# Performance work log

Hardware: AMD Instinct MI355X
Metric: run time of the kernel (lower is better)

The kernel has to match this reference:

```python
import jax, jax.numpy as jnp
import numpy as np

B, H, W, C = 8, 64, 64, 64
C8 = C // 8

def setup_inputs() -> dict:
    key = jax.random.key(0)
    ks = jax.random.split(key, 5)
    x = jax.random.normal(ks[0], (B, H, W, C), dtype=jnp.float32)
    # 1x1 conv kernels (fan-in scaled) + biases
    wq = jax.random.normal(ks[1], (C, C8), dtype=jnp.float32) / np.sqrt(C)
    wk = jax.random.normal(ks[2], (C, C8), dtype=jnp.float32) / np.sqrt(C)
    wv = jax.random.normal(ks[3], (C, C), dtype=jnp.float32) / np.sqrt(C)
    bq = jnp.zeros((C8,), dtype=jnp.float32)
    bk = jnp.zeros((C8,), dtype=jnp.float32)
    bv = jnp.zeros((C,), dtype=jnp.float32)
    gamma = jax.random.normal(ks[4], (), dtype=jnp.float32)
    return {"x": x, "wq": wq, "bq": bq, "wk": wk, "bk": bk,
            "wv": wv, "bv": bv, "gamma": gamma}

def reference(x, wq, bq, wk, bk, wv, bv, gamma):
    b, h, w, c = x.shape
    n = h * w
    # 1x1 convs == per-pixel linear projections
    q = (jnp.einsum('bhwc,cd->bhwd', x, wq) + bq).reshape(b, n, -1)  # [B,N,C/8]
    k = (jnp.einsum('bhwc,cd->bhwd', x, wk) + bk).reshape(b, n, -1)  # [B,N,C/8]
    v = (jnp.einsum('bhwc,cd->bhwd', x, wv) + bv).reshape(b, n, -1)  # [B,N,C]
    # Unscaled attention: softmax over keys (last axis), no 1/sqrt(d)
    attn = jax.nn.softmax(jnp.einsum('bnd,bmd->bnm', q, k), axis=-1)  # [B,N,N]
    out = jnp.einsum('bnm,bmc->bnc', attn, v).reshape(b, h, w, c)
    return out * gamma + x
```

## Files before the change

### kernel.cpp

```cpp
#include <hip/hip_runtime.h>
#include <hip/hip_bf16.h>


#define BB 8
#define NN 4096
#define CC 64
#define PSTRIDE 72
#define LOG2E 1.44269504088896f

typedef _Float16 f16;
typedef _Float16 half8 __attribute__((ext_vector_type(8)));
typedef _Float16 half4 __attribute__((ext_vector_type(4)));
typedef __fp16 fp16x2 __attribute__((ext_vector_type(2)));
typedef float floatx4 __attribute__((ext_vector_type(4)));

static __device__ inline half4 pack4(float a, float b, float c, float d) {
    fp16x2 lo = __builtin_amdgcn_cvt_pkrtz(a, b);
    fp16x2 hi = __builtin_amdgcn_cvt_pkrtz(c, d);
    unsigned int lou = __builtin_bit_cast(unsigned int, lo);
    unsigned int hiu = __builtin_bit_cast(unsigned int, hi);
    unsigned long long packed = (unsigned long long)lou | ((unsigned long long)hiu << 32);
    return __builtin_bit_cast(half4, packed);
}


__global__ __launch_bounds__(256) void proj_all_kernel(
    const float* __restrict__ x,
    const float* __restrict__ wq, const float* __restrict__ bq,
    const float* __restrict__ wk, const float* __restrict__ bk,
    const float* __restrict__ wv, const float* __restrict__ bv,
    f16* __restrict__ Qh, f16* __restrict__ Kf, f16* __restrict__ Vf,
    float* __restrict__ qn2, float* __restrict__ Mkb)
{
    __shared__ alignas(16) f16 Ws[80][PSTRIDE];
    __shared__ float Bs[80];
    __shared__ alignas(16) f16 Vst[64][68];
    __shared__ alignas(16) f16 Ks[64][12];
    __shared__ float redK[4];
    const int tid = threadIdx.x;

    for (int i4 = tid; i4 < 1024; i4 += 256) {
        const int i = i4 * 4;
        const int cin = i >> 6, cout = i & 63;
        const float4 w = *(const float4*)(wv + i);
        Ws[cout + 0][cin] = (f16)w.x;
        Ws[cout + 1][cin] = (f16)w.y;
        Ws[cout + 2][cin] = (f16)w.z;
        Ws[cout + 3][cin] = (f16)w.w;
    }
    if (tid < 128) {
        const int i = tid * 4;
        const int cin = i >> 3, c = i & 7;
        const float4 a = *(const float4*)(wq + i);
        const float4 k = *(const float4*)(wk + i);
        Ws[64 + c + 0][cin] = (f16)(a.x * LOG2E);
        Ws[64 + c + 1][cin] = (f16)(a.y * LOG2E);
        Ws[64 + c + 2][cin] = (f16)(a.z * LOG2E);
        Ws[64 + c + 3][cin] = (f16)(a.w * LOG2E);
        Ws[72 + c + 0][cin] = (f16)k.x;
        Ws[72 + c + 1][cin] = (f16)k.y;
        Ws[72 + c + 2][cin] = (f16)k.z;
        Ws[72 + c + 3][cin] = (f16)k.w;
    }
    if (tid < 80)
        Bs[tid] = (tid < 64) ? bv[tid]
                : (tid < 72 ? bq[tid - 64] * LOG2E : bk[tid - 72]);
    __syncthreads();

    const int wave = tid >> 6, lane = tid & 63;
    const int quad = lane >> 4, n16 = lane & 15;
    const long pb = (long)blockIdx.x * 64;
    const long p0 = pb + wave * 16;
    const int  b   = (int)(pb >> 12);
    const int  nnb = (int)(pb & 4095);

    half8 ax[2];
#pragma unroll
    for (int kh = 0; kh < 2; ++kh) {
        const float* xp = x + (p0 + n16) * 64 + kh * 32 + quad * 8;
        float4 x1 = *(const float4*)xp;
        float4 x2 = *(const float4*)(xp + 4);
        ax[kh][0] = (f16)x1.x; ax[kh][1] = (f16)x1.y;
        ax[kh][2] = (f16)x1.z; ax[kh][3] = (f16)x1.w;
        ax[kh][4] = (f16)x2.x; ax[kh][5] = (f16)x2.y;
        ax[kh][6] = (f16)x2.z; ax[kh][7] = (f16)x2.w;
    }

#pragma unroll
    for (int ct = 0; ct < 5; ++ct) {
        const int cout = (ct < 4) ? ct * 16 + n16 : 64 + n16;
        const float bias = Bs[cout];
        half8 b0 = *(const half8*)(&Ws[cout][quad * 8]);
        half8 b1 = *(const half8*)(&Ws[cout][32 + quad * 8]);
        floatx4 acc = {bias, bias, bias, bias};
        acc = __builtin_amdgcn_mfma_f32_16x16x32_f16(ax[0], b0, acc, 0, 0, 0);
        acc = __builtin_amdgcn_mfma_f32_16x16x32_f16(ax[1], b1, acc, 0, 0, 0);
        if (ct < 4) {
            half4 vp = {(f16)acc[0], (f16)acc[1], (f16)acc[2], (f16)acc[3]};
            *(half4*)(&Vst[ct * 16 + n16][wave * 16 + quad * 4]) = vp;
        } else {
            float n2[4];
#pragma unroll
            for (int r = 0; r < 4; ++r) n2[r] = acc[r] * acc[r];
#pragma unroll
            for (int d = 1; d < 8; d <<= 1)
#pragma unroll
                for (int r = 0; r < 4; ++r) n2[r] += __shfl_xor(n2[r], d, 64);
            if (n16 == 0) {
#pragma unroll
                for (int r = 0; r < 4; ++r) qn2[p0 + quad * 4 + r] = n2[r];
            }
            float km = fmaxf(fmaxf(n2[0], n2[1]), fmaxf(n2[2], n2[3]));
            km = fmaxf(km, __shfl_xor(km, 16, 64));
            km = fmaxf(km, __shfl_xor(km, 32, 64));
            if (n16 == 8) redK[wave] = km;
            if (n16 < 8) {
                f16* dst = Qh + (p0 + quad * 4) * 8 + n16;
#pragma unroll
                for (int r = 0; r < 4; ++r) dst[r * 8] = (f16)acc[r];
            } else {
#pragma unroll
                for (int r = 0; r < 4; ++r)
                    Ks[wave * 16 + quad * 4 + r][n16 - 8] = (f16)acc[r];
            }
        }
    }
    __syncthreads();

    if (tid == 0) {
        float m = fmaxf(fmaxf(redK[0], redK[1]), fmaxf(redK[2], redK[3]));
        Mkb[blockIdx.x] = m;
    }

#pragma unroll
    for (int u = 0; u < 2; ++u) {
        const int tt = wave * 2 + u;
        const int kb = tt >> 2, ct = tt & 3;
        half4 lo = *(const half4*)(&Vst[ct * 16 + n16][kb * 32 + quad * 4]);
        half4 hi = *(const half4*)(&Vst[ct * 16 + n16][kb * 32 + 16 + quad * 4]);
        half8 v = {lo[0], lo[1], lo[2], lo[3], hi[0], hi[1], hi[2], hi[3]};
        const size_t kbg = (size_t)b * 128 + (nnb >> 5) + kb;
        *(half8*)(Vf + (kbg * 4 + ct) * 512 + lane * 8) = v;
    }
    if (wave < 2) {
        half8 kp = {0, 0, 0, 0, 0, 0, 0, 0};
#pragma unroll
        for (int e = 0; e < 2; ++e) {
            const int t = wave * 2 + e;
            if (quad < 2) {
                half4 kd = *(const half4*)(&Ks[t * 16 + n16][quad * 4]);
                kp[e * 4 + 0] = kd[0]; kp[e * 4 + 1] = kd[1];
                kp[e * 4 + 2] = kd[2]; kp[e * 4 + 3] = kd[3];
            } else if (quad == 2) {
                kp[e * 4 + 0] = (f16)1.f;
            }
        }
        const size_t kpg = (size_t)b * 128 + (nnb >> 5) + wave;
        *(half8*)(Kf + kpg * 512 + lane * 8) = kp;
    }
}

__global__ __launch_bounds__(256, 3) void attn_kernel(
    const f16* __restrict__ Qh, const f16* __restrict__ Kf,
    const f16* __restrict__ Vf,
    const float* __restrict__ qn2, const float* __restrict__ Mkb,
    const float* __restrict__ x, const float* __restrict__ gptr,
    float* __restrict__ out)
{
    __shared__ alignas(16) char smem[30720];
    __shared__ float Ls[4][2][16];
    float* Obuf = (float*)smem;

    const int tid  = threadIdx.x;
    const int wave = tid >> 6, lane = tid & 63;
    const int quad = lane >> 4, n16 = lane & 15;
    const int ks = wave;

    const int b  = blockIdx.x & 7;
    const int qt = blockIdx.x >> 3;
    const size_t bN = (size_t)b * NN;

    float mk2;
    {
        float m = Mkb[b * 64 + lane];
        m = fmaxf(m, __shfl_xor(m, 1, 64));
        m = fmaxf(m, __shfl_xor(m, 2, 64));
        m = fmaxf(m, __shfl_xor(m, 4, 64));
        m = fmaxf(m, __shfl_xor(m, 8, 64));
        m = fmaxf(m, __shfl_xor(m, 16, 64));
        m = fmaxf(m, __shfl_xor(m, 32, 64));
        mk2 = m;
    }

    half4 bq4[2];
#pragma unroll
    for (int qt2 = 0; qt2 < 2; ++qt2) {
        const int q = qt * 32 + qt2 * 16 + n16;
        const float mf = __builtin_sqrtf(qn2[bN + q] * mk2) - 12.0f;
        half4 v = {0, 0, 0, 0};
        if (quad < 2)
            v = *(const half4*)(Qh + (bN + q) * 8 + quad * 4);
        else if (quad == 2)
            v[0] = (f16)(-mf);
        bq4[qt2] = v;
    }

    floatx4 oacc[2][4];
#pragma unroll
    for (int qt2 = 0; qt2 < 2; ++qt2)
#pragma unroll
        for (int ct = 0; ct < 4; ++ct) oacc[qt2][ct] = (floatx4){0.f, 0.f, 0.f, 0.f};
    float l_loc[2] = {0.f, 0.f};

    const f16* kfb = Kf + ((size_t)b * 128 + ks * 32) * 512 + lane * 8;
    const f16* vfb = Vf + ((size_t)b * 128 + ks * 32) * 2048 + lane * 8;
    const floatx4 zero4 = {0.f, 0.f, 0.f, 0.f};

    half8 kkc0 = *(const half8*)(kfb + 0);
    half8 kkc1 = *(const half8*)(kfb + 512);

    for (int it = 0; it < 16; ++it) {
        half8 avp[2][4];
#pragma unroll
        for (int p = 0; p < 2; ++p)
#pragma unroll
            for (int ct = 0; ct < 4; ++ct)
                avp[p][ct] = *(const half8*)(vfb + ((size_t)(it * 2 + p) * 4 + ct) * 512);

        half4 ak[4];
        ak[0] = __builtin_shufflevector(kkc0, kkc0, 0, 1, 2, 3);
        ak[1] = __builtin_shufflevector(kkc0, kkc0, 4, 5, 6, 7);
        ak[2] = __builtin_shufflevector(kkc1, kkc1, 0, 1, 2, 3);
        ak[3] = __builtin_shufflevector(kkc1, kkc1, 4, 5, 6, 7);

        const int itn = (it < 15) ? it + 1 : 15;
        kkc0 = *(const half8*)(kfb + (size_t)itn * 1024);
        kkc1 = *(const half8*)(kfb + (size_t)itn * 1024 + 512);

#pragma unroll
        for (int qt2 = 0; qt2 < 2; ++qt2) {
            floatx4 sf[4];
#pragma unroll
            for (int t = 0; t < 4; ++t)
                sf[t] = __builtin_amdgcn_mfma_f32_16x16x16f16(ak[t], bq4[qt2], zero4, 0, 0, 0);

            half4 pk[4];
            float rst[4];
#pragma unroll
            for (int t = 0; t < 4; ++t) {
                float p0 = __builtin_exp2f(sf[t][0]);
                float p1 = __builtin_exp2f(sf[t][1]);
                float p2 = __builtin_exp2f(sf[t][2]);
                float p3 = __builtin_exp2f(sf[t][3]);
                rst[t] = (p0 + p1) + (p2 + p3);
                pk[t] = pack4(p0, p1, p2, p3);
            }
            l_loc[qt2] += (rst[0] + rst[1]) + (rst[2] + rst[3]);

#pragma unroll
            for (int t = 0; t < 4; ++t) {
                const int p = t >> 1;
#pragma unroll
                for (int ct = 0; ct < 4; ++ct) {
                    half4 va = (t & 1)
                        ? __builtin_shufflevector(avp[p][ct], avp[p][ct], 4, 5, 6, 7)
                        : __builtin_shufflevector(avp[p][ct], avp[p][ct], 0, 1, 2, 3);
                    oacc[qt2][ct] = __builtin_amdgcn_mfma_f32_16x16x16f16(va, pk[t], oacc[qt2][ct], 0, 0, 0);
                }
            }
        }
    }

    float l_run[2];
#pragma unroll
    for (int qt2 = 0; qt2 < 2; ++qt2) {
        float l = l_loc[qt2];
        l += __shfl_xor(l, 16, 64);
        l += __shfl_xor(l, 32, 64);
        l_run[qt2] = l;
    }

    __syncthreads();
    if (ks > 0) {
#pragma unroll
        for (int qt2 = 0; qt2 < 2; ++qt2) {
            if (quad == 0) Ls[ks][qt2][n16] = l_run[qt2];
            float* ob = Obuf + (size_t)(((ks - 1) * 2 + qt2) * 64 + lane) * 20;
#pragma unroll
            for (int ct = 0; ct < 4; ++ct)
                *(floatx4*)(ob + ct * 4) = oacc[qt2][ct];
        }
    }
    __syncthreads();
    if (ks == 0) {
        const float g = gptr[0];
#pragma unroll
        for (int qt2 = 0; qt2 < 2; ++qt2) {
            float l = l_run[qt2];
            float o[16];
#pragma unroll
            for (int ct = 0; ct < 4; ++ct)
#pragma unroll
                for (int r = 0; r < 4; ++r) o[ct * 4 + r] = oacc[qt2][ct][r];
#pragma unroll
            for (int p = 1; p < 4; ++p) {
                l += Ls[p][qt2][n16];
                const float* ob = Obuf + (size_t)(((p - 1) * 2 + qt2) * 64 + lane) * 20;
#pragma unroll
                for (int ct = 0; ct < 4; ++ct) {
                    floatx4 t = *(const floatx4*)(ob + ct * 4);
                    o[ct * 4 + 0] += t[0]; o[ct * 4 + 1] += t[1];
                    o[ct * 4 + 2] += t[2]; o[ct * 4 + 3] += t[3];
                }
            }
            const float scale = g / l;
            const int q = qt * 32 + qt2 * 16 + n16;
#pragma unroll
            for (int ct = 0; ct < 4; ++ct) {
                const size_t idx = (bN + q) * CC + ct * 16 + quad * 4;
                float4 xr = *(const float4*)(x + idx);
                float4 res;
                res.x = o[ct * 4 + 0] * scale + xr.x;
                res.y = o[ct * 4 + 1] * scale + xr.y;
                res.z = o[ct * 4 + 2] * scale + xr.z;
                res.w = o[ct * 4 + 3] * scale + xr.w;
                *(float4*)(out + idx) = res;
            }
        }
    }
}

extern "C" void kernel_launch(void* const* d_in, const int* in_sizes, int n_in,
                              void* d_out, int out_size, void* d_ws, size_t ws_size,
                              hipStream_t stream) {
    const float* x     = (const float*)d_in[0];
    const float* wq    = (const float*)d_in[1];
    const float* bq    = (const float*)d_in[2];
    const float* wk    = (const float*)d_in[3];
    const float* bk    = (const float*)d_in[4];
    const float* wv    = (const float*)d_in[5];
    const float* bv    = (const float*)d_in[6];
    const float* gamma = (const float*)d_in[7];
    float* out = (float*)d_out;

    f16* Qh = (f16*)d_ws;
    f16* Kf = Qh + (size_t)BB * NN * 8;
    f16* Vf = Kf + (size_t)BB * 128 * 512;
    float* qn2 = (float*)(Vf + (size_t)BB * 128 * 4 * 512);
    float* Mkb = qn2 + (size_t)BB * NN;

    proj_all_kernel<<<512, 256, 0, stream>>>(x, wq, bq, wk, bk, wv, bv,
                                             Qh, Kf, Vf, qn2, Mkb);
    attn_kernel<<<BB * 128, 256, 0, stream>>>(Qh, Kf, Vf, qn2, Mkb, x, gamma, out);
}
```

Baseline: 122.6 us.

## Double-buffer K/V tile loads with inline asm and explicit vmcnt waits

Replaces the attention main loop with an explicitly double-buffered pipeline. Each tile's K and V fragments are issued as inline-asm global_load_dwordx4 into two register sets, and s_waitcnt vmcnt(10) waits only for the older tile. Before, only K was prefetched and V was loaded at the top of each iteration, which could stall the MFMA chain. In exchange it roughly doubles the registers held for V, which may lower occupancy at launch bounds of 3 waves per SIMD. The hand-written waitcnt also takes correctness away from the compiler.

```diff
diff --git a/kernel.cpp b/kernel.cpp
--- a/kernel.cpp
+++ b/kernel.cpp
@@ -160,6 +160,73 @@
     }
 }
 
+
+#define XC(M, ...) M(__VA_ARGS__)
+
+#define ISSUE_TILE(ITN, K0, K1, V00, V01, V02, V03, V10, V11, V12, V13) do { \
+    const char* kb_  = kfb + (size_t)(ITN) * 2048;                            \
+    const char* vb0_ = vfb + (size_t)(ITN) * 8192;                            \
+    const char* vb1_ = vb0_ + 4096;                                           \
+    __asm__ volatile("global_load_dwordx4 %0, %1, off"             : "=&v"(K0)  : "v"(kb_)  : "memory"); \
+    __asm__ volatile("global_load_dwordx4 %0, %1, off offset:1024" : "=&v"(K1)  : "v"(kb_)  : "memory"); \
+    __asm__ volatile("global_load_dwordx4 %0, %1, off"             : "=&v"(V00) : "v"(vb0_) : "memory"); \
+    __asm__ volatile("global_load_dwordx4 %0, %1, off offset:1024" : "=&v"(V01) : "v"(vb0_) : "memory"); \
+    __asm__ volatile("global_load_dwordx4 %0, %1, off offset:2048" : "=&v"(V02) : "v"(vb0_) : "memory"); \
+    __asm__ volatile("global_load_dwordx4 %0, %1, off offset:3072" : "=&v"(V03) : "v"(vb0_) : "memory"); \
+    __asm__ volatile("global_load_dwordx4 %0, %1, off"             : "=&v"(V10) : "v"(vb1_) : "memory"); \
+    __asm__ volatile("global_load_dwordx4 %0, %1, off offset:1024" : "=&v"(V11) : "v"(vb1_) : "memory"); \
+    __asm__ volatile("global_load_dwordx4 %0, %1, off offset:2048" : "=&v"(V12) : "v"(vb1_) : "memory"); \
+    __asm__ volatile("global_load_dwordx4 %0, %1, off offset:3072" : "=&v"(V13) : "v"(vb1_) : "memory"); \
+} while (0)
+
+#define WAIT_TILE(CNT, K0, K1, V00, V01, V02, V03, V10, V11, V12, V13)        \
+    __asm__ volatile("s_waitcnt vmcnt(" CNT ")"                               \
+        : "+v"(K0), "+v"(K1), "+v"(V00), "+v"(V01), "+v"(V02), "+v"(V03),     \
+          "+v"(V10), "+v"(V11), "+v"(V12), "+v"(V13) :: "memory")
+
+#define SM_PV(SF, HI, VA, VB, VC, VD) do {                                    \
+    float p0_ = __builtin_exp2f((SF)[0]);                                     \
+    float p1_ = __builtin_exp2f((SF)[1]);                                     \
+    float p2_ = __builtin_exp2f((SF)[2]);                                     \
+    float p3_ = __builtin_exp2f((SF)[3]);                                     \
+    l_loc[qt2] += (p0_ + p1_) + (p2_ + p3_);                                  \
+    half4 pk_ = pack4(p0_, p1_, p2_, p3_);                                    \
+    half4 va_;                                                                \
+    va_ = (HI) ? __builtin_shufflevector(VA, VA, 4, 5, 6, 7)                  \
+               : __builtin_shufflevector(VA, VA, 0, 1, 2, 3);                 \
+    oacc[qt2][0] = __builtin_amdgcn_mfma_f32_16x16x16f16(va_, pk_, oacc[qt2][0], 0, 0, 0); \
+    va_ = (HI) ? __builtin_shufflevector(VB, VB, 4, 5, 6, 7)                  \
+               : __builtin_shufflevector(VB, VB, 0, 1, 2, 3);                 \
+    oacc[qt2][1] = __builtin_amdgcn_mfma_f32_16x16x16f16(va_, pk_, oacc[qt2][1], 0, 0, 0); \
+    va_ = (HI) ? __builtin_shufflevector(VC, VC, 4, 5, 6, 7)                  \
+               : __builtin_shufflevector(VC, VC, 0, 1, 2, 3);                 \
+    oacc[qt2][2] = __builtin_amdgcn_mfma_f32_16x16x16f16(va_, pk_, oacc[qt2][2], 0, 0, 0); \
+    va_ = (HI) ? __builtin_shufflevector(VD, VD, 4, 5, 6, 7)                  \
+               : __builtin_shufflevector(VD, VD, 0, 1, 2, 3);                 \
+    oacc[qt2][3] = __builtin_amdgcn_mfma_f32_16x16x16f16(va_, pk_, oacc[qt2][3], 0, 0, 0); \
+} while (0)
+
+#define COMPUTE_TILE(K0, K1, V00, V01, V02, V03, V10, V11, V12, V13) do {     \
+    half4 ak0_ = __builtin_shufflevector(K0, K0, 0, 1, 2, 3);                 \
+    half4 ak1_ = __builtin_shufflevector(K0, K0, 4, 5, 6, 7);                 \
+    half4 ak2_ = __builtin_shufflevector(K1, K1, 0, 1, 2, 3);                 \
+    half4 ak3_ = __builtin_shufflevector(K1, K1, 4, 5, 6, 7);                 \
+    _Pragma("unroll")                                                         \
+    for (int qt2 = 0; qt2 < 2; ++qt2) {                                       \
+        floatx4 sf0_ = __builtin_amdgcn_mfma_f32_16x16x16f16(ak0_, bq4[qt2], zero4, 0, 0, 0); \
+        floatx4 sf1_ = __builtin_amdgcn_mfma_f32_16x16x16f16(ak1_, bq4[qt2], zero4, 0, 0, 0); \
+        floatx4 sf2_ = __builtin_amdgcn_mfma_f32_16x16x16f16(ak2_, bq4[qt2], zero4, 0, 0, 0); \
+        floatx4 sf3_ = __builtin_amdgcn_mfma_f32_16x16x16f16(ak3_, bq4[qt2], zero4, 0, 0, 0); \
+        SM_PV(sf0_, 0, V00, V01, V02, V03);                                   \
+        SM_PV(sf1_, 1, V00, V01, V02, V03);                                   \
+        SM_PV(sf2_, 0, V10, V11, V12, V13);                                   \
+        SM_PV(sf3_, 1, V10, V11, V12, V13);                                   \
+    }                                                                         \
+} while (0)
+
+#define AREGS kA0, kA1, vA00, vA01, vA02, vA03, vA10, vA11, vA12, vA13
+#define BREGS kB0, kB1, vB00, vB01, vB02, vB03, vB10, vB11, vB12, vB13
+
 __global__ __launch_bounds__(256, 3) void attn_kernel(
     const f16* __restrict__ Qh, const f16* __restrict__ Kf,
     const f16* __restrict__ Vf,
@@ -212,64 +279,27 @@
         for (int ct = 0; ct < 4; ++ct) oacc[qt2][ct] = (floatx4){0.f, 0.f, 0.f, 0.f};
     float l_loc[2] = {0.f, 0.f};
 
-    const f16* kfb = Kf + ((size_t)b * 128 + ks * 32) * 512 + lane * 8;
-    const f16* vfb = Vf + ((size_t)b * 128 + ks * 32) * 2048 + lane * 8;
+    const char* kfb = (const char*)(Kf + ((size_t)b * 128 + ks * 32) * 512 + lane * 8);
+    const char* vfb = (const char*)(Vf + ((size_t)b * 128 + ks * 32) * 2048 + lane * 8);
     const floatx4 zero4 = {0.f, 0.f, 0.f, 0.f};
 
-    half8 kkc0 = *(const half8*)(kfb + 0);
-    half8 kkc1 = *(const half8*)(kfb + 512);
-
-    for (int it = 0; it < 16; ++it) {
-        half8 avp[2][4];
-#pragma unroll
-        for (int p = 0; p < 2; ++p)
-#pragma unroll
-            for (int ct = 0; ct < 4; ++ct)
-                avp[p][ct] = *(const half8*)(vfb + ((size_t)(it * 2 + p) * 4 + ct) * 512);
-
-        half4 ak[4];
-        ak[0] = __builtin_shufflevector(kkc0, kkc0, 0, 1, 2, 3);
-        ak[1] = __builtin_shufflevector(kkc0, kkc0, 4, 5, 6, 7);
-        ak[2] = __builtin_shufflevector(kkc1, kkc1, 0, 1, 2, 3);
-        ak[3] = __builtin_shufflevector(kkc1, kkc1, 4, 5, 6, 7);
-
-        const int itn = (it < 15) ? it + 1 : 15;
-        kkc0 = *(const half8*)(kfb + (size_t)itn * 1024);
-        kkc1 = *(const half8*)(kfb + (size_t)itn * 1024 + 512);
-
-#pragma unroll
-        for (int qt2 = 0; qt2 < 2; ++qt2) {
-            floatx4 sf[4];
-#pragma unroll
-            for (int t = 0; t < 4; ++t)
-                sf[t] = __builtin_amdgcn_mfma_f32_16x16x16f16(ak[t], bq4[qt2], zero4, 0, 0, 0);
-
-            half4 pk[4];
-            float rst[4];
-#pragma unroll
-            for (int t = 0; t < 4; ++t) {
-                float p0 = __builtin_exp2f(sf[t][0]);
-                float p1 = __builtin_exp2f(sf[t][1]);
-                float p2 = __builtin_exp2f(sf[t][2]);
-                float p3 = __builtin_exp2f(sf[t][3]);
-                rst[t] = (p0 + p1) + (p2 + p3);
-                pk[t] = pack4(p0, p1, p2, p3);
-            }
-            l_loc[qt2] += (rst[0] + rst[1]) + (rst[2] + rst[3]);
-
-#pragma unroll
-            for (int t = 0; t < 4; ++t) {
-                const int p = t >> 1;
-#pragma unroll
-                for (int ct = 0; ct < 4; ++ct) {
-                    half4 va = (t & 1)
-                        ? __builtin_shufflevector(avp[p][ct], avp[p][ct], 4, 5, 6, 7)
-                        : __builtin_shufflevector(avp[p][ct], avp[p][ct], 0, 1, 2, 3);
-                    oacc[qt2][ct] = __builtin_amdgcn_mfma_f32_16x16x16f16(va, pk[t], oacc[qt2][ct], 0, 0, 0);
-                }
-            }
-        }
-    }
+    half8 kA0, kA1, vA00, vA01, vA02, vA03, vA10, vA11, vA12, vA13;
+    half8 kB0, kB1, vB00, vB01, vB02, vB03, vB10, vB11, vB12, vB13;
+
+    XC(ISSUE_TILE, 0, AREGS);
+    for (int i2 = 0; i2 < 7; ++i2) {
+        XC(ISSUE_TILE, 2 * i2 + 1, BREGS);
+        XC(WAIT_TILE, "10", AREGS);
+        XC(COMPUTE_TILE, AREGS);
+        XC(ISSUE_TILE, 2 * i2 + 2, AREGS);
+        XC(WAIT_TILE, "10", BREGS);
+        XC(COMPUTE_TILE, BREGS);
+    }
+    XC(ISSUE_TILE, 15, BREGS);
+    XC(WAIT_TILE, "10", AREGS);
+    XC(COMPUTE_TILE, AREGS);
+    XC(WAIT_TILE, "0", BREGS);
+    XC(COMPUTE_TILE, BREGS);
 
     float l_run[2];
 #pragma unroll
```

After: 125.0 us. About the same (+2.0%).
